# Kernel tuning notes

Hardware: AMD Instinct MI355X
Metric: run time of the kernel (lower is better)

The kernel has to match this reference:

```python
import jax, jax.numpy as jnp
import numpy as np

BLOCK_M, BLOCK_K = 16, 64
THRES = 0.8


def setup_inputs() -> dict:
    key = jax.random.key(0)
    kx, kw = jax.random.split(key)
    bsz, seq, in_f, out_f = 128, 1, 4096, 11008
    x = jax.random.normal(kx, (bsz, seq, in_f), dtype=jnp.float16)
    # kaiming_uniform_(a=sqrt(5)) on a (in,out) weight -> bound = 1/sqrt(fan_in)
    bound = 1.0 / np.sqrt(in_f)
    weight = jax.random.uniform(kw, (in_f, out_f), dtype=jnp.float16,
                                minval=-bound, maxval=bound)
    bias = jnp.zeros((out_f,), dtype=jnp.float16)
    return {"x": x, "weight": weight, "bias": bias}


def reference(x, weight, bias):
    bsz, seq, hidden = x.shape
    x2 = x.reshape(bsz * seq, hidden)          # (M, K), seq == 1 decode path
    M, K = x2.shape
    # avg_magnitude_threshold: per (BLOCK_M, BLOCK_K) block mean |x| vs thres
    blocks = x2.reshape(M // BLOCK_M, BLOCK_M, K // BLOCK_K, BLOCK_K)
    avg = jnp.mean(jnp.abs(blocks).astype(jnp.float32), axis=(1, 3))  # (M/bm, K/bk)
    mask = avg > THRES                           # block active if avg magnitude above thres
    # blocksparse_masked_gemm: skipped blocks contribute nothing -> zero them out
    xm = jnp.where(mask[:, None, :, None], blocks, jnp.float16(0)).reshape(M, K)
    y = xm @ weight                              # (M, out_features)
    return y.reshape(bsz, seq, -1) + bias
```

## Files before the change

kernel.cpp:

```cpp
#include <hip/hip_runtime.h>
#include <stdint.h>

using f32x4   = __attribute__((ext_vector_type(4))) float;
using short8  = __attribute__((ext_vector_type(8))) short;
using float2v = __attribute__((ext_vector_type(2))) float;
using uint4v  = __attribute__((ext_vector_type(4))) unsigned int;

#define NCOL 11008
#define KDIM 4096
#define KSEG 4
#define KB_PER_SEG 16
#define TILE_B 8192

#define AS1 __attribute__((address_space(1)))
#define AS3 __attribute__((address_space(3)))

__device__ __forceinline__ unsigned pk_bf16(float a, float b) {
  unsigned ua = __float_as_uint(a); ua += 0x7fffu + ((ua >> 16) & 1u);
  unsigned ub = __float_as_uint(b); ub += 0x7fffu + ((ub >> 16) & 1u);
  return (ua >> 16) | (ub & 0xffff0000u);
}

__global__ __launch_bounds__(256) void mask_convert_kernel(
    const float* __restrict__ x, unsigned* __restrict__ xbf) {
  const int rb = blockIdx.x;
  const int g  = blockIdx.y;
  const int t  = threadIdx.x;
  __shared__ double part[256];
  __shared__ unsigned sh_bits;

  const float* base = x + (size_t)rb * 16 * KDIM + g * 512 + t * 2;
  double s = 0.0;
#pragma unroll
  for (int r = 0; r < 16; ++r) {
    float2v a = *(const float2v*)(base + (size_t)r * KDIM);
    s += (double)fabsf(a[0]) + (double)fabsf(a[1]);
  }
  part[t] = s;
  __syncthreads();
  if (t < 8) {
    double acc = 0.0;
#pragma unroll
    for (int u = 0; u < 32; ++u) acc += part[t * 32 + u];
    bool on = (acc * (1.0 / 1024.0)) > (double)0.8f;
    unsigned long long bal = __ballot(on);
    if (t == 0) sh_bits = (unsigned)(bal & 0xffu);
  }
  __syncthreads();
  const unsigned keep = (sh_bits >> (t >> 5)) & 1u;

  unsigned* dst = xbf + (size_t)rb * 16 * (KDIM / 2) + g * 256 + t;
#pragma unroll
  for (int r = 0; r < 16; ++r) {
    float2v a = *(const float2v*)(base + (size_t)r * KDIM);
    dst[(size_t)r * (KDIM / 2)] = keep ? pk_bf16(a[0], a[1]) : 0u;
  }
}

__global__ __launch_bounds__(256) void bias_init_kernel(
    const float* __restrict__ bias, float* __restrict__ out) {
  const int n = blockIdx.x * 256 + threadIdx.x;
  out[(size_t)blockIdx.y * NCOL + n] = bias[n];
}

__global__ __launch_bounds__(256) void gemm_kernel(
    const unsigned* __restrict__ xbf, const float* __restrict__ w,
    float* __restrict__ out) {

  __shared__ __align__(16) uint8_t lds[2 * TILE_B];

  const int tid  = threadIdx.x;
  const int lane = tid & 63;
  const int wv   = tid >> 6;
  const int c    = lane & 15;
  const int q    = lane >> 4;
  const int n0   = blockIdx.x * 32;
  const int kb0  = blockIdx.y * KB_PER_SEG;

  f32x4 acc[2][2] = {};

  const int kA = tid >> 3;
  const int cB = (tid & 7) * 4;
  const float* gW = w + (size_t)kA * NCOL + n0 + cB;

#define STAGE(PBUF, KBI)                                                     \
  {                                                                          \
    const float* g_ = gW + (size_t)(KBI) * 64 * NCOL;                        \
    __builtin_amdgcn_global_load_lds(                                        \
        (const AS1 void*)g_,                                                 \
        (AS3 void*)(lds + (PBUF) * TILE_B + wv * 1024), 16, 0, 0);           \
    __builtin_amdgcn_global_load_lds(                                        \
        (const AS1 void*)(g_ + (size_t)32 * NCOL),                           \
        (AS3 void*)(lds + (PBUF) * TILE_B + 4096 + wv * 1024), 16, 0, 0);    \
  }

  const uint4v* aB0 = (const uint4v*)xbf + (size_t)((wv * 2 + 0) * 16 + c) * (KDIM / 8) + q;
  const uint4v* aB1 = (const uint4v*)xbf + (size_t)((wv * 2 + 1) * 16 + c) * (KDIM / 8) + q;

  auto compute = [&](const uint8_t* buf, int kbi) {
    union { uint4v u; short8 v; } a00, a01, a10, a11;
    a00.u = aB0[kbi * 8 + 0];
    a01.u = aB0[kbi * 8 + 4];
    a10.u = aB1[kbi * 8 + 0];
    a11.u = aB1[kbi * 8 + 4];

#pragma unroll
    for (int ks = 0; ks < 2; ++ks) {
      const uint8_t* wb = buf + (size_t)(ks * 32 + q * 8) * 128 + c * 8;
      float2v r[8];
#pragma unroll
      for (int j = 0; j < 8; ++j)
        r[j] = *(const float2v*)(wb + (size_t)j * 128);
      union { short8 v; unsigned u[4]; } be, bo;
#pragma unroll
      for (int p = 0; p < 4; ++p) {
        be.u[p] = pk_bf16(r[2 * p][0], r[2 * p + 1][0]);
        bo.u[p] = pk_bf16(r[2 * p][1], r[2 * p + 1][1]);
      }
      const short8 a0 = ks ? a01.v : a00.v;
      const short8 a1 = ks ? a11.v : a10.v;
      acc[0][0] = __builtin_amdgcn_mfma_f32_16x16x32_bf16(a0, be.v, acc[0][0], 0, 0, 0);
      acc[0][1] = __builtin_amdgcn_mfma_f32_16x16x32_bf16(a0, bo.v, acc[0][1], 0, 0, 0);
      acc[1][0] = __builtin_amdgcn_mfma_f32_16x16x32_bf16(a1, be.v, acc[1][0], 0, 0, 0);
      acc[1][1] = __builtin_amdgcn_mfma_f32_16x16x32_bf16(a1, bo.v, acc[1][1], 0, 0, 0);
    }
  };

  STAGE(0, kb0);
  __syncthreads();

  int p = 0;
  for (int i = 0; i < KB_PER_SEG; ++i) {
    if (i + 1 < KB_PER_SEG) STAGE(p ^ 1, kb0 + i + 1);
    compute(lds + p * TILE_B, kb0 + i);
    __syncthreads();
    p ^= 1;
  }
#undef STAGE

  const int colE = n0 + 2 * c;
#pragma unroll
  for (int b = 0; b < 2; ++b) {
#pragma unroll
    for (int pp = 0; pp < 4; ++pp) {
      const int row = (wv * 2 + b) * 16 + q * 4 + pp;
      float* pdst = out + (size_t)row * NCOL + colE;
      __hip_atomic_fetch_add(pdst,     acc[b][0][pp], __ATOMIC_RELAXED,
                             __HIP_MEMORY_SCOPE_AGENT);
      __hip_atomic_fetch_add(pdst + 1, acc[b][1][pp], __ATOMIC_RELAXED,
                             __HIP_MEMORY_SCOPE_AGENT);
    }
  }
}

extern "C" void kernel_launch(void* const* d_in, const int* in_sizes, int n_in,
                              void* d_out, int out_size, void* d_ws, size_t ws_size,
                              hipStream_t stream) {
  const float* x    = (const float*)d_in[0];
  const float* w    = (const float*)d_in[1];
  const float* bias = (const float*)d_in[2];
  float* out        = (float*)d_out;
  unsigned* xbf     = (unsigned*)d_ws;

  hipLaunchKernelGGL(mask_convert_kernel, dim3(8, 8), dim3(256), 0, stream, x, xbf);
  hipLaunchKernelGGL(bias_init_kernel, dim3(43, 128), dim3(256), 0, stream, bias, out);
  hipLaunchKernelGGL(gemm_kernel, dim3(344, KSEG), dim3(256), 0, stream,
                     xbf, w, out);
}
```

Measured before the change: 288.7 us.

## Widen GEMM tiles to 256 columns with 512-thread blocks and deeper K split

The GEMM is retiled so each 512-thread block covers 256 output columns by all 128 rows. Each weight row slice is a contiguous 1 KB strip staged into LDS with global_load_lds, and every wave issues 16 MFMAs per stage against four A fragments. This is meant to improve weight-load coalescing and raise compute per staged byte over the previous 32-column tiles. The split-K factor doubles from 4 to 8, which doubles the fp32 atomic adds to the output. It also uses 64 KB of double-buffered LDS per block and launches far fewer blocks, which may reduce occupancy and load balance.

After: 325.3 us. 1.13x slower.

```diff
diff --git a/kernel.cpp b/kernel.cpp
--- a/kernel.cpp
+++ b/kernel.cpp
@@ -8,9 +8,9 @@
 
 #define NCOL 11008
 #define KDIM 4096
-#define KSEG 4
-#define KB_PER_SEG 16
-#define TILE_B 8192
+#define KSPLIT 8
+#define PHASES 16
+#define TILE_B 32768
 
 #define AS1 __attribute__((address_space(1)))
 #define AS3 __attribute__((address_space(3)))
@@ -63,7 +63,7 @@
   out[(size_t)blockIdx.y * NCOL + n] = bias[n];
 }
 
-__global__ __launch_bounds__(256) void gemm_kernel(
+__global__ __launch_bounds__(512, 4) void gemm_kernel(
     const unsigned* __restrict__ xbf, const float* __restrict__ w,
     float* __restrict__ out) {
 
@@ -74,81 +74,83 @@
   const int wv   = tid >> 6;
   const int c    = lane & 15;
   const int q    = lane >> 4;
-  const int n0   = blockIdx.x * 32;
-  const int kb0  = blockIdx.y * KB_PER_SEG;
+  const int mg   = wv >> 2;
+  const int ng   = wv & 3;
+  const int n0   = blockIdx.x * 256;
+  const int k0b  = blockIdx.y * 512;
 
-  f32x4 acc[2][2] = {};
+  f32x4 acc[4][2][2] = {};
 
-  const int kA = tid >> 3;
-  const int cB = (tid & 7) * 4;
-  const float* gW = w + (size_t)kA * NCOL + n0 + cB;
+  const float* gW = w + n0 + lane * 4;
 
-#define STAGE(PBUF, KBI)                                                     \
-  {                                                                          \
-    const float* g_ = gW + (size_t)(KBI) * 64 * NCOL;                        \
-    __builtin_amdgcn_global_load_lds(                                        \
-        (const AS1 void*)g_,                                                 \
-        (AS3 void*)(lds + (PBUF) * TILE_B + wv * 1024), 16, 0, 0);           \
-    __builtin_amdgcn_global_load_lds(                                        \
-        (const AS1 void*)(g_ + (size_t)32 * NCOL),                           \
-        (AS3 void*)(lds + (PBUF) * TILE_B + 4096 + wv * 1024), 16, 0, 0);    \
+#define STAGE(BUF, K0)                                                      \
+  {                                                                         \
+    _Pragma("unroll")                                                       \
+    for (int r_ = 0; r_ < 4; ++r_) {                                        \
+      __builtin_amdgcn_global_load_lds(                                     \
+          (const AS1 void*)(gW + (size_t)((K0) + r_ * 8 + wv) * NCOL),      \
+          (AS3 void*)((BUF) + r_ * 8192 + wv * 1024), 16, 0, 0);            \
+    }                                                                       \
   }
 
-  const uint4v* aB0 = (const uint4v*)xbf + (size_t)((wv * 2 + 0) * 16 + c) * (KDIM / 8) + q;
-  const uint4v* aB1 = (const uint4v*)xbf + (size_t)((wv * 2 + 1) * 16 + c) * (KDIM / 8) + q;
+  const uint4v* aBase = (const uint4v*)xbf;
 
-  auto compute = [&](const uint8_t* buf, int kbi) {
-    union { uint4v u; short8 v; } a00, a01, a10, a11;
-    a00.u = aB0[kbi * 8 + 0];
-    a01.u = aB0[kbi * 8 + 4];
-    a10.u = aB1[kbi * 8 + 0];
-    a11.u = aB1[kbi * 8 + 4];
+  auto compute = [&](const uint8_t* buf, int k0) {
+    union { uint4v u; short8 v; } a[4];
+#pragma unroll
+    for (int fm = 0; fm < 4; ++fm)
+      a[fm].u = aBase[(size_t)(mg * 64 + fm * 16 + c) * 512 + (k0 >> 3) + q];
 
 #pragma unroll
-    for (int ks = 0; ks < 2; ++ks) {
-      const uint8_t* wb = buf + (size_t)(ks * 32 + q * 8) * 128 + c * 8;
-      float2v r[8];
-#pragma unroll
-      for (int j = 0; j < 8; ++j)
-        r[j] = *(const float2v*)(wb + (size_t)j * 128);
+    for (int g = 0; g < 2; ++g) {
+      const uint8_t* wb = buf + ng * 256 + g * 128 + c * 8;
       union { short8 v; unsigned u[4]; } be, bo;
 #pragma unroll
       for (int p = 0; p < 4; ++p) {
-        be.u[p] = pk_bf16(r[2 * p][0], r[2 * p + 1][0]);
-        bo.u[p] = pk_bf16(r[2 * p][1], r[2 * p + 1][1]);
+        float2v f0 = *(const float2v*)(wb + (size_t)(q * 8 + 2 * p) * 1024);
+        float2v f1 = *(const float2v*)(wb + (size_t)(q * 8 + 2 * p + 1) * 1024);
+        be.u[p] = pk_bf16(f0[0], f1[0]);
+        bo.u[p] = pk_bf16(f0[1], f1[1]);
       }
-      const short8 a0 = ks ? a01.v : a00.v;
-      const short8 a1 = ks ? a11.v : a10.v;
-      acc[0][0] = __builtin_amdgcn_mfma_f32_16x16x32_bf16(a0, be.v, acc[0][0], 0, 0, 0);
-      acc[0][1] = __builtin_amdgcn_mfma_f32_16x16x32_bf16(a0, bo.v, acc[0][1], 0, 0, 0);
-      acc[1][0] = __builtin_amdgcn_mfma_f32_16x16x32_bf16(a1, be.v, acc[1][0], 0, 0, 0);
-      acc[1][1] = __builtin_amdgcn_mfma_f32_16x16x32_bf16(a1, bo.v, acc[1][1], 0, 0, 0);
+#pragma unroll
+      for (int fm = 0; fm < 4; ++fm) {
+        acc[fm][g][0] = __builtin_amdgcn_mfma_f32_16x16x32_bf16(a[fm].v, be.v, acc[fm][g][0], 0, 0, 0);
+        acc[fm][g][1] = __builtin_amdgcn_mfma_f32_16x16x32_bf16(a[fm].v, bo.v, acc[fm][g][1], 0, 0, 0);
+      }
     }
   };
 
-  STAGE(0, kb0);
+  uint8_t* const buf0 = lds;
+  uint8_t* const buf1 = lds + TILE_B;
+
+  STAGE(buf0, k0b);
   __syncthreads();
 
   int p = 0;
-  for (int i = 0; i < KB_PER_SEG; ++i) {
-    if (i + 1 < KB_PER_SEG) STAGE(p ^ 1, kb0 + i + 1);
-    compute(lds + p * TILE_B, kb0 + i);
+  for (int ph = 0; ph < PHASES; ++ph) {
+    uint8_t* cur = p ? buf1 : buf0;
+    uint8_t* nxt = p ? buf0 : buf1;
+    if (ph + 1 < PHASES) STAGE(nxt, k0b + (ph + 1) * 32);
+    compute(cur, k0b + ph * 32);
     __syncthreads();
     p ^= 1;
   }
 #undef STAGE
 
-  const int colE = n0 + 2 * c;
+  const int colE = n0 + ng * 64 + 2 * c;
 #pragma unroll
-  for (int b = 0; b < 2; ++b) {
+  for (int fm = 0; fm < 4; ++fm) {
 #pragma unroll
-    for (int pp = 0; pp < 4; ++pp) {
-      const int row = (wv * 2 + b) * 16 + q * 4 + pp;
-      float* pdst = out + (size_t)row * NCOL + colE;
-      __hip_atomic_fetch_add(pdst,     acc[b][0][pp], __ATOMIC_RELAXED,
-                             __HIP_MEMORY_SCOPE_AGENT);
-      __hip_atomic_fetch_add(pdst + 1, acc[b][1][pp], __ATOMIC_RELAXED,
-                             __HIP_MEMORY_SCOPE_AGENT);
+    for (int g = 0; g < 2; ++g) {
+#pragma unroll
+      for (int pp = 0; pp < 4; ++pp) {
+        const int row = mg * 64 + fm * 16 + q * 4 + pp;
+        float* pd = out + (size_t)row * NCOL + colE + g * 32;
+        __hip_atomic_fetch_add(pd,     acc[fm][g][0][pp], __ATOMIC_RELAXED,
+                               __HIP_MEMORY_SCOPE_AGENT);
+        __hip_atomic_fetch_add(pd + 1, acc[fm][g][1][pp], __ATOMIC_RELAXED,
+                               __HIP_MEMORY_SCOPE_AGENT);
+      }
     }
   }
 }
@@ -164,6 +166,6 @@
 
   hipLaunchKernelGGL(mask_convert_kernel, dim3(8, 8), dim3(256), 0, stream, x, xbf);
   hipLaunchKernelGGL(bias_init_kernel, dim3(43, 128), dim3(256), 0, stream, bias, out);
-  hipLaunchKernelGGL(gemm_kernel, dim3(344, KSEG), dim3(256), 0, stream,
+  hipLaunchKernelGGL(gemm_kernel, dim3(43, KSPLIT), dim3(512), 0, stream,
                      xbf, w, out);
 }
```

## Stage activations through a swizzled LDS ring with three-deep async prefetch

Applied to the files above, without the earlier changes.

The bf16 activation tiles are now fetched asynchronously into LDS with global_load_lds, next to the weight tiles, using an XOR swizzle on the 16-byte slots to avoid bank conflicts. Previously they were read straight from global memory inside compute. Double buffering becomes a three-slot ring with explicit vmcnt waits and one barrier per iteration instead of a trailing __syncthreads. The goal is to hide activation load latency and cut synchronisation stalls. The cost is much more LDS per block (72 KB instead of 16 KB), which limits how many blocks fit on a CU.

Result: no change. 287.5 us (-0.4%).

```diff
diff --git a/kernel.cpp b/kernel.cpp
--- a/kernel.cpp
+++ b/kernel.cpp
@@ -10,7 +10,7 @@
 #define KDIM 4096
 #define KSEG 4
 #define KB_PER_SEG 16
-#define TILE_B 8192
+#define RING_B 24576
 
 #define AS1 __attribute__((address_space(1)))
 #define AS3 __attribute__((address_space(3)))
@@ -67,7 +67,7 @@
     const unsigned* __restrict__ xbf, const float* __restrict__ w,
     float* __restrict__ out) {
 
-  __shared__ __align__(16) uint8_t lds[2 * TILE_B];
+  __shared__ __align__(16) uint8_t lds[3 * RING_B];
 
   const int tid  = threadIdx.x;
   const int lane = tid & 63;
@@ -83,29 +83,46 @@
   const int cB = (tid & 7) * 4;
   const float* gW = w + (size_t)kA * NCOL + n0 + cB;
 
-#define STAGE(PBUF, KBI)                                                     \
-  {                                                                          \
-    const float* g_ = gW + (size_t)(KBI) * 64 * NCOL;                        \
-    __builtin_amdgcn_global_load_lds(                                        \
-        (const AS1 void*)g_,                                                 \
-        (AS3 void*)(lds + (PBUF) * TILE_B + wv * 1024), 16, 0, 0);           \
-    __builtin_amdgcn_global_load_lds(                                        \
-        (const AS1 void*)(g_ + (size_t)32 * NCOL),                           \
-        (AS3 void*)(lds + (PBUF) * TILE_B + 4096 + wv * 1024), 16, 0, 0);    \
+  const unsigned swz = ((unsigned)(lane & 7) ^ (unsigned)(lane >> 3)) << 4;
+  const uint8_t* gA = (const uint8_t*)xbf + swz;
+
+#define ISSUE_GROUP(RB, KBI)                                                  \
+  {                                                                           \
+    uint8_t* base_ = lds + (RB) * RING_B;                                     \
+    const float* g_ = gW + (size_t)(KBI) * 64 * NCOL;                         \
+    __builtin_amdgcn_global_load_lds((const AS1 void*)g_,                     \
+        (AS3 void*)(base_ + wv * 1024), 16, 0, 0);                            \
+    __builtin_amdgcn_global_load_lds((const AS1 void*)(g_ + (size_t)32*NCOL), \
+        (AS3 void*)(base_ + 4096 + wv * 1024), 16, 0, 0);                     \
+    _Pragma("unroll")                                                         \
+    for (int t_ = 0; t_ < 4; ++t_) {                                          \
+      const int r_ = wv * 32 + t_ * 8 + (lane >> 3);                          \
+      __builtin_amdgcn_global_load_lds(                                       \
+          (const AS1 void*)(gA + (size_t)r_ * 8192 + (size_t)(KBI) * 128),    \
+          (AS3 void*)(base_ + 8192 + wv * 4096 + t_ * 1024), 16, 0, 0);       \
+    }                                                                         \
   }
 
-  const uint4v* aB0 = (const uint4v*)xbf + (size_t)((wv * 2 + 0) * 16 + c) * (KDIM / 8) + q;
-  const uint4v* aB1 = (const uint4v*)xbf + (size_t)((wv * 2 + 1) * 16 + c) * (KDIM / 8) + q;
+#define WAITV(N)                                                              \
+  { asm volatile("s_waitcnt vmcnt(" #N ")" ::: "memory");                     \
+    __builtin_amdgcn_sched_barrier(0); }
+#define BAR()                                                                 \
+  { asm volatile("s_waitcnt lgkmcnt(0)" ::: "memory");                        \
+    __builtin_amdgcn_s_barrier(); __builtin_amdgcn_sched_barrier(0); }
 
-  auto compute = [&](const uint8_t* buf, int kbi) {
-    union { uint4v u; short8 v; } a00, a01, a10, a11;
-    a00.u = aB0[kbi * 8 + 0];
-    a01.u = aB0[kbi * 8 + 4];
-    a10.u = aB1[kbi * 8 + 0];
-    a11.u = aB1[kbi * 8 + 4];
-
+  auto compute = [&](const uint8_t* buf) {
+    const uint8_t* Ab = buf + 8192;
 #pragma unroll
     for (int ks = 0; ks < 2; ++ks) {
+      union { uint4v u; short8 v; } a0, a1;
+      {
+        const int row0 = (wv * 2 + 0) * 16 + c;
+        const int row1 = (wv * 2 + 1) * 16 + c;
+        const int sl0 = (ks * 4 + q) ^ (row0 & 7);
+        const int sl1 = (ks * 4 + q) ^ (row1 & 7);
+        a0.u = *(const uint4v*)(Ab + (size_t)row0 * 128 + sl0 * 16);
+        a1.u = *(const uint4v*)(Ab + (size_t)row1 * 128 + sl1 * 16);
+      }
       const uint8_t* wb = buf + (size_t)(ks * 32 + q * 8) * 128 + c * 8;
       float2v r[8];
 #pragma unroll
@@ -117,26 +134,29 @@
         be.u[p] = pk_bf16(r[2 * p][0], r[2 * p + 1][0]);
         bo.u[p] = pk_bf16(r[2 * p][1], r[2 * p + 1][1]);
       }
-      const short8 a0 = ks ? a01.v : a00.v;
-      const short8 a1 = ks ? a11.v : a10.v;
-      acc[0][0] = __builtin_amdgcn_mfma_f32_16x16x32_bf16(a0, be.v, acc[0][0], 0, 0, 0);
-      acc[0][1] = __builtin_amdgcn_mfma_f32_16x16x32_bf16(a0, bo.v, acc[0][1], 0, 0, 0);
-      acc[1][0] = __builtin_amdgcn_mfma_f32_16x16x32_bf16(a1, be.v, acc[1][0], 0, 0, 0);
-      acc[1][1] = __builtin_amdgcn_mfma_f32_16x16x32_bf16(a1, bo.v, acc[1][1], 0, 0, 0);
+      acc[0][0] = __builtin_amdgcn_mfma_f32_16x16x32_bf16(a0.v, be.v, acc[0][0], 0, 0, 0);
+      acc[0][1] = __builtin_amdgcn_mfma_f32_16x16x32_bf16(a0.v, bo.v, acc[0][1], 0, 0, 0);
+      acc[1][0] = __builtin_amdgcn_mfma_f32_16x16x32_bf16(a1.v, be.v, acc[1][0], 0, 0, 0);
+      acc[1][1] = __builtin_amdgcn_mfma_f32_16x16x32_bf16(a1.v, bo.v, acc[1][1], 0, 0, 0);
     }
   };
 
-  STAGE(0, kb0);
-  __syncthreads();
+  ISSUE_GROUP(0, kb0);
 
-  int p = 0;
-  for (int i = 0; i < KB_PER_SEG; ++i) {
-    if (i + 1 < KB_PER_SEG) STAGE(p ^ 1, kb0 + i + 1);
-    compute(lds + p * TILE_B, kb0 + i);
-    __syncthreads();
-    p ^= 1;
+#pragma unroll
+  for (int j = 0; j < KB_PER_SEG; ++j) {
+    if (j + 1 < KB_PER_SEG) {
+      ISSUE_GROUP((j + 1) % 3, kb0 + j + 1);
+      WAITV(6);
+    } else {
+      WAITV(0);
+    }
+    BAR();
+    compute(lds + (j % 3) * RING_B);
   }
-#undef STAGE
+#undef ISSUE_GROUP
+#undef WAITV
+#undef BAR
 
   const int colE = n0 + 2 * c;
 #pragma unroll
```
